# Kernel tuning notes

Measured on AMD Instinct MI355X. Metric: run time of the kernel, lower is better.

The kernel has to match this reference:

```python
import jax, jax.numpy as jnp
import numpy as np

B, N, C, H = 2, 2048, 256, 8
HD = C // H
LN_EPS = 1e-5
BN_EPS = 1e-5  # eval-mode BatchNorm with running_mean=0, running_var=1


def _ln(x, g, b):
    # LayerNorm over last dim
    m = jnp.mean(x, axis=-1, keepdims=True)
    v = jnp.mean((x - m) ** 2, axis=-1, keepdims=True)
    return (x - m) * jax.lax.rsqrt(v + LN_EPS) * g + b


def _ln_cn(x, g, b):
    # x: [B,C,N], normalize over C (torch does transpose -> LN -> transpose)
    return jnp.swapaxes(_ln(jnp.swapaxes(x, 1, 2), g, b), 1, 2)


def _cdist(a, b):
    # a: [B,N,D], b: [B,M,D] -> [B,N,M] euclidean
    d2 = (jnp.sum(a * a, -1)[:, :, None] + jnp.sum(b * b, -1)[:, None, :]
          - 2.0 * jnp.einsum('bnd,bmd->bnm', a, b))
    return jnp.sqrt(jnp.maximum(d2, 0.0))


def _conv1x1(w, x, b=None):
    # w: [O,C], x: [B,C,N]
    y = jnp.einsum('oc,bcn->bon', w, x)
    return y if b is None else y + b[None, :, None]


def setup_inputs() -> dict:
    key = jax.random.key(0)
    ks = jax.random.split(key, 32)
    s = 0.02
    inp = {
        'xyz_A': jax.random.normal(ks[0], (B, N, 3), jnp.float32),
        'featA': jax.random.normal(ks[1], (B, C, N), jnp.float32),
        'xyz_B': jax.random.normal(ks[2], (B, N, 3), jnp.float32),
        'featB': jax.random.normal(ks[3], (B, C, N), jnp.float32),
        'ln_in_g': jnp.ones((C,), jnp.float32),
        'ln_in_b': jnp.zeros((C,), jnp.float32),
        'Wq': jax.random.normal(ks[4], (C, C), jnp.float32) * s,
        'bq': jnp.zeros((C,), jnp.float32),
        'Wk': jax.random.normal(ks[5], (C, C), jnp.float32) * s,
        'bk': jnp.zeros((C,), jnp.float32),
        'Wv': jax.random.normal(ks[6], (C, C), jnp.float32) * s,
        'bv': jnp.zeros((C,), jnp.float32),
        'sb_w1': jax.random.normal(ks[7], (H // 2, 1), jnp.float32) * s,
        'sb_bn_g': jnp.ones((H // 2,), jnp.float32),
        'sb_bn_b': jnp.zeros((H // 2,), jnp.float32),
        'sb_w2': jax.random.normal(ks[8], (H, H // 2), jnp.float32) * s,
        'sb_b2': jnp.zeros((H,), jnp.float32),
        'Wqd': jax.random.normal(ks[9], (C, C), jnp.float32) * s,
        'bqd': jnp.zeros((C,), jnp.float32),
        'Wkd': jax.random.normal(ks[10], (C, C), jnp.float32) * s,
        'bkd': jnp.zeros((C,), jnp.float32),
        'ln_sim_g': jnp.ones((C,), jnp.float32),
        'ln_sim_b': jnp.zeros((C,), jnp.float32),
        'ln_dis_g': jnp.ones((C,), jnp.float32),
        'ln_dis_b': jnp.zeros((C,), jnp.float32),
        'Wf1': jax.random.normal(ks[11], (2 * C, 3 * C), jnp.float32) * s,
        'bnf_g': jnp.ones((2 * C,), jnp.float32),
        'bnf_b': jnp.zeros((2 * C,), jnp.float32),
        'Wf2': jax.random.normal(ks[12], (C, 2 * C), jnp.float32) * s,
        'bf2': jnp.zeros((C,), jnp.float32),
    }
    return inp


def reference(xyz_A, featA, xyz_B, featB, ln_in_g, ln_in_b, Wq, bq, Wk, bk, Wv, bv,
              sb_w1, sb_bn_g, sb_bn_b, sb_w2, sb_b2, Wqd, bqd, Wkd, bkd,
              ln_sim_g, ln_sim_b, ln_dis_g, ln_dis_b, Wf1, bnf_g, bnf_b, Wf2, bf2):
    featA_norm = _ln_cn(featA, ln_in_g, ln_in_b)  # [B,C,N]

    # spatial bias: cdist -> 1x1 conv2d MLP over channel dim
    dist = _cdist(xyz_A, xyz_B)  # [B,N,N]
    h = jnp.einsum('oi,binm->bonm', sb_w1, -dist[:, None])  # [B,H/2,N,N]
    h = h * (sb_bn_g / np.sqrt(1.0 + BN_EPS))[None, :, None, None] + sb_bn_b[None, :, None, None]
    h = jax.nn.relu(h)
    spatial_bias = jnp.einsum('oi,binm->bonm', sb_w2, h) + sb_b2[None, :, None, None]  # [B,H,N,N]

    # similarity path
    q = _conv1x1(Wq, featA_norm, bq).reshape(B, H, HD, N).transpose(0, 1, 3, 2)  # [B,H,N,hd]
    k = _conv1x1(Wk, featB, bk).reshape(B, H, HD, N).transpose(0, 1, 3, 2)
    sim_scores = jnp.einsum('bhnd,bhmd->bhnm', q, k) / np.sqrt(HD) + spatial_bias

    # dissimilarity path: feature-space cdist
    qd = jnp.swapaxes(_conv1x1(Wqd, featA_norm, bqd), 1, 2)  # [B,N,C]
    kd = jnp.swapaxes(_conv1x1(Wkd, featB, bkd), 1, 2)
    dissim_scores = _cdist(qd, kd)[:, None] + spatial_bias  # [B,H,N,N]

    sim_w = jax.nn.softmax(sim_scores, axis=-1)
    dis_w = jax.nn.softmax(dissim_scores, axis=-1)

    v = _conv1x1(Wv, featB, bv).reshape(B, H, HD, N).transpose(0, 1, 3, 2)  # [B,H,N,hd]
    ctx_sim = jnp.einsum('bhnm,bhmd->bhnd', sim_w, v).transpose(0, 1, 3, 2).reshape(B, C, N)
    ctx_sim = _ln_cn(ctx_sim, ln_sim_g, ln_sim_b)
    ctx_dis = jnp.einsum('bhnm,bhmd->bhnd', dis_w, v).transpose(0, 1, 3, 2).reshape(B, C, N)
    ctx_dis = _ln_cn(ctx_dis, ln_dis_g, ln_dis_b)

    fused_in = jnp.concatenate([featA_norm, ctx_sim, ctx_dis], axis=1)  # [B,3C,N]
    f = jnp.einsum('oc,bcn->bon', Wf1, fused_in)
    f = f * (bnf_g / np.sqrt(1.0 + BN_EPS))[None, :, None] + bnf_b[None, :, None]
    f = jax.nn.relu(f)
    fused = jnp.einsum('oc,bcn->bon', Wf2, f) + bf2[None, :, None]

    return fused + featA  # residual (in_channel == out_channel -> Identity)
```

## Files before the change

kernel.cpp:

```cpp
#include <hip/hip_runtime.h>
#include <math.h>

#define B_ 2
#define N_ 2048
#define C_ 256
#define H_ 8
#define HD_ 32
constexpr float LN_EPS_ = 1e-5f;
constexpr float BN_EPS_ = 1e-5f;
constexpr float LOG2E_ = 1.4426950408889634f;
constexpr float ISDL_ = 0.17677669529663687f * 1.4426950408889634f;

typedef __attribute__((ext_vector_type(8))) short bf16x8;
typedef __attribute__((ext_vector_type(4))) float f32x4;

static __device__ inline ushort f2bf(float x) {
    union { float f; uint u; } c{x};
    uint r = (c.u + 0x7FFF + ((c.u >> 16) & 1)) >> 16;
    return (ushort)r;
}
static __device__ inline float bf2f(ushort u) {
    union { uint i; float f; } c; c.i = ((uint)u) << 16; return c.f;
}
static __device__ inline float bf_lo(uint u) { return __uint_as_float(u << 16); }
static __device__ inline float bf_hi(uint u) { return __uint_as_float(u & 0xffff0000u); }
static __device__ inline float lane_bcast(float v, int srclane) {
    return __int_as_float(__builtin_amdgcn_ds_bpermute(srclane * 4, __float_as_int(v)));
}
static __device__ inline uint pack_bf2(float lo, float hi) {
    uint ul = __float_as_uint(lo) + 0x8000u;
    uint uh = __float_as_uint(hi) + 0x8000u;
    return __builtin_amdgcn_perm(uh, ul, 0x07060302u);
}

__global__ __launch_bounds__(256)
void k_wconv(const float* __restrict__ Wq, const float* __restrict__ Wqd,
             const float* __restrict__ Wk, const float* __restrict__ Wkd,
             const float* __restrict__ Wv, const float* __restrict__ Wf1,
             const float* __restrict__ Wf2, ushort* __restrict__ dst)
{
    size_t e0 = ((size_t)blockIdx.x * 256 + threadIdx.x) * 8;
    const float* src = Wq; size_t base = 0;
    if (e0 >= 65536)  { src = Wqd; base = 65536; }
    if (e0 >= 131072) { src = Wk;  base = 131072; }
    if (e0 >= 196608) { src = Wkd; base = 196608; }
    if (e0 >= 262144) { src = Wv;  base = 262144; }
    if (e0 >= 327680) { src = Wf1; base = 327680; }
    if (e0 >= 720896) { src = Wf2; base = 720896; }
    float4 a = *(const float4*)(src + (e0 - base));
    float4 b = *(const float4*)(src + (e0 - base) + 4);
    ushort o[8] = {f2bf(a.x), f2bf(a.y), f2bf(a.z), f2bf(a.w),
                   f2bf(b.x), f2bf(b.y), f2bf(b.z), f2bf(b.w)};
    *(uint4*)(dst + e0) = *(uint4*)o;
}

__global__ __launch_bounds__(512)
void k_bconcat(const float* __restrict__ bq, const float* __restrict__ bqd,
               const float* __restrict__ bk, const float* __restrict__ bkd,
               float* __restrict__ bqqd, float* __restrict__ bkkd)
{
    int t = threadIdx.x;
    bqqd[t] = (t < 256) ? bq[t] : bqd[t - 256];
    bkkd[t] = (t < 256) ? bk[t] : bkd[t - 256];
}

template<bool DO_LN>
__global__ __launch_bounds__(256)
void k_ln_transpose(const float* __restrict__ x,
                    const float* __restrict__ g,
                    const float* __restrict__ bt,
                    ushort* __restrict__ out, int ld)
{
    __shared__ float tile[C_][65];
    __shared__ float red_s[4][64];
    __shared__ float red_q[4][64];
    __shared__ float ms[64];
    __shared__ float rs[64];

    const int b  = blockIdx.x / (N_ / 64);
    const int n0 = (blockIdx.x % (N_ / 64)) * 64;
    const int tid = threadIdx.x;

    for (int i = 0; i < 64; ++i) {
        int c = i * 4 + (tid >> 6);
        int n = tid & 63;
        tile[c][n] = x[((size_t)b * C_ + c) * N_ + n0 + n];
    }
    __syncthreads();

    float gv = 0.f, bv = 0.f;
    if (DO_LN) { gv = g[tid]; bv = bt[tid]; }

    if (DO_LN) {
        const int nl = tid & 63, part = tid >> 6;
        float s = 0.f, q = 0.f;
        for (int j = 0; j < 64; ++j) {
            float v = tile[part * 64 + j][nl];
            s += v; q += v * v;
        }
        red_s[part][nl] = s; red_q[part][nl] = q;
        __syncthreads();
        if (tid < 64) {
            float ss = red_s[0][tid] + red_s[1][tid] + red_s[2][tid] + red_s[3][tid];
            float qq = red_q[0][tid] + red_q[1][tid] + red_q[2][tid] + red_q[3][tid];
            float mean = ss * (1.0f / C_);
            float var  = qq * (1.0f / C_) - mean * mean;
            ms[tid] = mean;
            rs[tid] = rsqrtf(var + LN_EPS_);
        }
        __syncthreads();
    }

    for (int i = 0; i < 64; ++i) {
        float v = tile[tid][i];
        if (DO_LN) v = (v - ms[i]) * rs[i] * gv + bv;
        out[((size_t)b * N_ + n0 + i) * ld + tid] = f2bf(v);
    }
}

template<int EPI, int OUT>
__global__ __launch_bounds__(256)
void k_gemm_bf(const ushort* __restrict__ A, int lda, size_t sAz,
               const ushort* __restrict__ Bw, int ldb, size_t sBz,
               void* __restrict__ Cout_, int ldc, size_t sCz,
               int K,
               const float* __restrict__ aux1,
               const float* __restrict__ aux2)
{
    const int z = blockIdx.z;
    A  += (size_t)z * sAz;
    Bw += (size_t)z * sBz;

    const int r0 = blockIdx.x * 64;
    const int c0 = blockIdx.y * 64;
    const int tid = threadIdx.x;
    const int w = tid >> 6, lane = tid & 63;
    const int wr = w >> 1, wc = w & 1;
    const int ql = lane & 15, g = lane >> 4;

    __shared__ ushort As[64][40];
    __shared__ ushort Bs[64][40];

    f32x4 acc[2][2] = {};
    const int srow = tid >> 2;
    const int sk   = (tid & 3) * 8;

    for (int k0 = 0; k0 < K; k0 += 32) {
        bf16x8 av = *(const bf16x8*)&A[(size_t)(r0 + srow) * lda + k0 + sk];
        bf16x8 bv = *(const bf16x8*)&Bw[(size_t)(c0 + srow) * ldb + k0 + sk];
        __syncthreads();
        *(bf16x8*)&As[srow][sk] = av;
        *(bf16x8*)&Bs[srow][sk] = bv;
        __syncthreads();
        bf16x8 af[2], bf[2];
        #pragma unroll
        for (int i = 0; i < 2; ++i) {
            af[i] = *(const bf16x8*)&As[wr * 32 + i * 16 + ql][8 * g];
            bf[i] = *(const bf16x8*)&Bs[wc * 32 + i * 16 + ql][8 * g];
        }
        #pragma unroll
        for (int mi = 0; mi < 2; ++mi)
            #pragma unroll
            for (int ni = 0; ni < 2; ++ni)
                acc[mi][ni] = __builtin_amdgcn_mfma_f32_16x16x32_bf16(af[mi], bf[ni], acc[mi][ni], 0, 0, 0);
    }

    const float inv_bn = rsqrtf(1.0f + BN_EPS_);
    float*  Cf = (float*)Cout_  + (size_t)z * sCz;
    ushort* Cb = (ushort*)Cout_ + (size_t)z * sCz;
    #pragma unroll
    for (int mi = 0; mi < 2; ++mi) {
        #pragma unroll
        for (int ni = 0; ni < 2; ++ni) {
            #pragma unroll
            for (int r = 0; r < 4; ++r) {
                int row = r0 + wr * 32 + mi * 16 + 4 * g + r;
                int col = c0 + wc * 32 + ni * 16 + ql;
                float v = acc[mi][ni][r];
                if (EPI == 0) {
                    v += aux1[col];
                } else if (EPI == 1) {
                    float qnv = aux1[(size_t)z * N_ + row];
                    float knv = aux2[(size_t)z * N_ + col];
                    v = sqrtf(fmaxf(qnv + knv - 2.0f * v, 0.f)) * LOG2E_;
                } else if (EPI == 2) {
                    v = fmaxf(v * (aux1[col] * inv_bn) + aux2[col], 0.f);
                } else if (EPI == 3) {
                    v += aux1[row];
                }
                if (OUT == 0) Cf[(size_t)row * ldc + col] = v;
                else          Cb[(size_t)row * ldc + col] = f2bf(v);
            }
        }
    }
}

__global__ __launch_bounds__(256)
void k_rownorm(const ushort* __restrict__ x, int ld, float* __restrict__ outn)
{
    const int r = blockIdx.x * 4 + (threadIdx.x >> 6);
    const int lane = threadIdx.x & 63;
    uint2 pv = *(const uint2*)&x[(size_t)r * ld + lane * 4];
    float v0 = bf2f((ushort)(pv.x & 0xffff)), v1 = bf2f((ushort)(pv.x >> 16));
    float v2 = bf2f((ushort)(pv.y & 0xffff)), v3 = bf2f((ushort)(pv.y >> 16));
    float s = v0 * v0 + v1 * v1 + v2 * v2 + v3 * v3;
    #pragma unroll
    for (int off = 32; off; off >>= 1) s += __shfl_xor(s, off);
    if (lane == 0) outn[r] = s;
}

#define QLD_ 512
__global__ __launch_bounds__(512, 4)
void k_attn7(const ushort* __restrict__ q_bf,
             const ushort* __restrict__ k_bf,
             const ushort* __restrict__ v_c,
             const float* __restrict__ xyzA,
             const float* __restrict__ xyzB,
             const ushort* __restrict__ cdb,
             const float* __restrict__ sb_w1, const float* __restrict__ sb_bn_g,
             const float* __restrict__ sb_bn_b, const float* __restrict__ sb_w2,
             const float* __restrict__ sb_b2,
             ushort* __restrict__ pc,
             float* __restrict__ pml)
{
    __shared__ ushort biasL[2][4][16][72];
    __shared__ ushort cdsL[2][16][72];
    __shared__ ushort ps[8][16][72];
    __shared__ float  w2Ls[4][4];
    __shared__ float  b2Ls[4];

    const int n0 = blockIdx.x * 16;
    const int b  = blockIdx.y;
    const int hg   = blockIdx.z & 1;
    const int half = blockIdx.z >> 1;
    const size_t bN = (size_t)b * N_;
    const int tid = threadIdx.x;
    const int w = tid >> 6, lane = tid & 63;
    const int path = w >> 2, hl = w & 3;
    const int h = hg * 4 + hl;
    const int ql = lane & 15, g = lane >> 4;

    if (tid < 4) {
        b2Ls[tid] = sb_b2[hg * 4 + tid] * LOG2E_;
        #pragma unroll
        for (int i = 0; i < 4; ++i) w2Ls[tid][i] = sb_w2[(hg * 4 + tid) * 4 + i] * LOG2E_;
    }

    const float inv_bn = rsqrtf(1.0f + BN_EPS_);
    float w1s_[4], bnb_[4];
    #pragma unroll
    for (int i = 0; i < 4; ++i) {
        w1s_[i] = sb_w1[i] * sb_bn_g[i] * inv_bn;
        bnb_[i] = sb_bn_b[i];
    }

    const int cq = tid >> 5, cm2 = tid & 31;
    const float ax = xyzA[(bN + n0 + cq) * 3 + 0];
    const float ay = xyzA[(bN + n0 + cq) * 3 + 1];
    const float az = xyzA[(bN + n0 + cq) * 3 + 2];

    bf16x8 qfrag = {};
    if (path == 0)
        qfrag = *(const bf16x8*)&q_bf[(bN + n0 + ql) * QLD_ + h * 32 + 8 * g];

    float m_i = -INFINITY, l_i = 0.f;
    f32x4 ctx0 = {0.f, 0.f, 0.f, 0.f};
    f32x4 ctx1 = {0.f, 0.f, 0.f, 0.f};
    const f32x4 zf = {0.f, 0.f, 0.f, 0.f};

    const int tBeg = half * (N_ / 128);
    const int tEnd = tBeg + (N_ / 128);

    float xb[6]; uint cdv;
    auto coop_load = [&](int t) {
        const int mA = t * 64 + 2 * cm2;
        const float* pb = xyzB + (bN + mA) * 3;
        #pragma unroll
        for (int i = 0; i < 6; ++i) xb[i] = pb[i];
        cdv = *(const uint*)&cdb[(bN + n0 + cq) * (size_t)N_ + mA];
    };
    auto coop_write = [&](int buf) {
        float dx0 = ax - xb[0], dy0 = ay - xb[1], dz0 = az - xb[2];
        float dx1 = ax - xb[3], dy1 = ay - xb[4], dz1 = az - xb[5];
        float d0 = sqrtf(dx0 * dx0 + dy0 * dy0 + dz0 * dz0);
        float d1 = sqrtf(dx1 * dx1 + dy1 * dy1 + dz1 * dz1);
        float f0[4], f1[4];
        #pragma unroll
        for (int i = 0; i < 4; ++i) {
            f0[i] = fmaxf(fmaf(-w1s_[i], d0, bnb_[i]), 0.f);
            f1[i] = fmaxf(fmaf(-w1s_[i], d1, bnb_[i]), 0.f);
        }
        #pragma unroll
        for (int hh = 0; hh < 4; ++hh) {
            const f32x4 w2v = *(const f32x4*)w2Ls[hh];
            float b0 = b2Ls[hh], b1 = b2Ls[hh];
            #pragma unroll
            for (int i = 0; i < 4; ++i) {
                b0 = fmaf(w2v[i], f0[i], b0);
                b1 = fmaf(w2v[i], f1[i], b1);
            }
            *(uint*)&biasL[buf][hh][cq][2 * cm2] = pack_bf2(b0, b1);
        }
        *(uint*)&cdsL[buf][cq][2 * cm2] = cdv;
    };

    __syncthreads();
    coop_load(tBeg);
    coop_write(0);
    if (tBeg + 1 < tEnd) coop_load(tBeg + 1);
    __syncthreads();

    for (int t = tBeg; t < tEnd; ++t) {
        const int cur = (t - tBeg) & 1;

        if (t + 1 < tEnd) {
            coop_write(cur ^ 1);
            if (t + 2 < tEnd) coop_load(t + 2);
        }

        const int m0 = t * 64;
        bf16x8 af[4];
        if (path == 0) {
            #pragma unroll
            for (int mt = 0; mt < 4; ++mt)
                af[mt] = *(const bf16x8*)&k_bf[(bN + m0 + mt * 16 + ql) * QLD_ + h * 32 + 8 * g];
        }
        bf16x8 vb[2][2];
        #pragma unroll
        for (int kb = 0; kb < 2; ++kb)
            #pragma unroll
            for (int dt = 0; dt < 2; ++dt)
                vb[kb][dt] = *(const bf16x8*)&v_c[((size_t)b * C_ + h * 32 + dt * 16 + ql) * N_ + m0 + kb * 32 + 8 * g];

        float s[16];
        #pragma unroll
        for (int mt = 0; mt < 4; ++mt) {
            uint2 bw = *(const uint2*)&biasL[cur][hl][ql][16 * mt + 4 * g];
            s[4 * mt + 0] = bf_lo(bw.x);
            s[4 * mt + 1] = bf_hi(bw.x);
            s[4 * mt + 2] = bf_lo(bw.y);
            s[4 * mt + 3] = bf_hi(bw.y);
        }

        if (path == 0) {
            __builtin_amdgcn_s_setprio(1);
            #pragma unroll
            for (int mt = 0; mt < 4; ++mt) {
                f32x4 sf = __builtin_amdgcn_mfma_f32_16x16x32_bf16(af[mt], qfrag, zf, 0, 0, 0);
                #pragma unroll
                for (int r = 0; r < 4; ++r)
                    s[4 * mt + r] = fmaf(sf[r], ISDL_, s[4 * mt + r]);
            }
            __builtin_amdgcn_s_setprio(0);
        } else {
            #pragma unroll
            for (int mt = 0; mt < 4; ++mt) {
                uint2 cw = *(const uint2*)&cdsL[cur][ql][16 * mt + 4 * g];
                s[4 * mt + 0] += bf_lo(cw.x);
                s[4 * mt + 1] += bf_hi(cw.x);
                s[4 * mt + 2] += bf_lo(cw.y);
                s[4 * mt + 3] += bf_hi(cw.y);
            }
        }

        float t0 = fmaxf(s[0], s[1]),   t1 = fmaxf(s[2], s[3]);
        float t2 = fmaxf(s[4], s[5]),   t3 = fmaxf(s[6], s[7]);
        float t4 = fmaxf(s[8], s[9]),   t5 = fmaxf(s[10], s[11]);
        float t6 = fmaxf(s[12], s[13]), t7 = fmaxf(s[14], s[15]);
        t0 = fmaxf(t0, t1); t2 = fmaxf(t2, t3);
        t4 = fmaxf(t4, t5); t6 = fmaxf(t6, t7);
        float tmax = fmaxf(fmaxf(t0, t2), fmaxf(t4, t6));
        tmax = fmaxf(tmax, __shfl_xor(tmax, 16));
        tmax = fmaxf(tmax, __shfl_xor(tmax, 32));
        if (!__all(tmax <= m_i + 8.0f)) {
            float mnew = fmaxf(m_i, tmax);
            float scl = exp2f(m_i - mnew);
            l_i *= scl;
            #pragma unroll
            for (int r = 0; r < 4; ++r) {
                float sr = lane_bcast(scl, 4 * g + r);
                ctx0[r] *= sr; ctx1[r] *= sr;
            }
            m_i = mnew;
        }
        float lsum = 0.f;
        #pragma unroll
        for (int j = 0; j < 16; ++j) {
            float pj = exp2f(s[j] - m_i);
            s[j] = pj;
            lsum += pj;
        }
        lsum += __shfl_xor(lsum, 16);
        lsum += __shfl_xor(lsum, 32);
        l_i += lsum;

        #pragma unroll
        for (int mt = 0; mt < 4; ++mt) {
            uint2 pk;
            pk.x = pack_bf2(s[4 * mt + 0], s[4 * mt + 1]);
            pk.y = pack_bf2(s[4 * mt + 2], s[4 * mt + 3]);
            *(uint2*)&ps[w][ql][16 * mt + 4 * g] = pk;
        }

        __builtin_amdgcn_s_setprio(1);
        #pragma unroll
        for (int kb = 0; kb < 2; ++kb) {
            bf16x8 pa = *(const bf16x8*)&ps[w][ql][kb * 32 + 8 * g];
            ctx0 = __builtin_amdgcn_mfma_f32_16x16x32_bf16(pa, vb[kb][0], ctx0, 0, 0, 0);
            ctx1 = __builtin_amdgcn_mfma_f32_16x16x32_bf16(pa, vb[kb][1], ctx1, 0, 0, 0);
        }
        __builtin_amdgcn_s_setprio(0);

        __syncthreads();
    }

    const size_t sl = (size_t)(half * 2 + path) * (B_ * N_);
    #pragma unroll
    for (int r = 0; r < 4; ++r) {
        size_t base = (sl + bN + n0 + 4 * g + r) * C_ + h * 32;
        pc[base + ql]      = f2bf(ctx0[r]);
        pc[base + 16 + ql] = f2bf(ctx1[r]);
    }
    if (g == 0) {
        size_t mlb = ((sl + bN + n0 + ql) * H_ + h) * 2;
        pml[mlb]     = m_i;
        pml[mlb + 1] = l_i;
    }
}

__global__ __launch_bounds__(256)
void k_merge_ln(const ushort* __restrict__ pc, const float* __restrict__ pml,
                const float* __restrict__ g_sim, const float* __restrict__ b_sim,
                const float* __restrict__ g_dis, const float* __restrict__ b_dis,
                ushort* __restrict__ fused_bf)
{
    __shared__ float rs_[4], rq_[4];
    const int row = blockIdx.x;
    const int path = blockIdx.y;
    const int c = threadIdx.x;
    const int h = c >> 5;
    const size_t i0 = (size_t)(0 * 2 + path) * (B_ * N_) + row;
    const size_t i1 = (size_t)(1 * 2 + path) * (B_ * N_) + row;
    const float m0 = pml[(i0 * H_ + h) * 2], l0 = pml[(i0 * H_ + h) * 2 + 1];
    const float m1 = pml[(i1 * H_ + h) * 2], l1 = pml[(i1 * H_ + h) * 2 + 1];
    const float M = fmaxf(m0, m1);
    const float w0 = exp2f(m0 - M), w1 = exp2f(m1 - M);
    const float il = 1.0f / fmaf(l0, w0, l1 * w1);
    const float v = fmaf(bf2f(pc[i0 * C_ + c]), w0, bf2f(pc[i1 * C_ + c]) * w1) * il;

    float s = v, q = v * v;
    #pragma unroll
    for (int off = 32; off; off >>= 1) { s += __shfl_xor(s, off); q += __shfl_xor(q, off); }
    const int wv = c >> 6, lane = c & 63;
    if (lane == 0) { rs_[wv] = s; rq_[wv] = q; }
    __syncthreads();
    float ss = rs_[0] + rs_[1] + rs_[2] + rs_[3];
    float qq = rq_[0] + rq_[1] + rq_[2] + rq_[3];
    float mean = ss * (1.0f / C_);
    float var  = qq * (1.0f / C_) - mean * mean;
    float rstd = rsqrtf(var + LN_EPS_);
    const float* gp = path ? g_dis : g_sim;
    const float* bp = path ? b_dis : b_sim;
    fused_bf[(size_t)row * (3 * C_) + C_ + path * C_ + c] =
        f2bf((v - mean) * rstd * gp[c] + bp[c]);
}

__global__ __launch_bounds__(256)
void k_transpose_add(const float* __restrict__ fused_t,
                     const float* __restrict__ featA,
                     float* __restrict__ out)
{
    __shared__ float t[64][65];
    const int n0 = blockIdx.x * 64, c0 = blockIdx.y * 64, b = blockIdx.z;
    const int tid = threadIdx.x;
    #pragma unroll
    for (int i = 0; i < 16; ++i) {
        int e = i * 256 + tid;
        int nn = e >> 6, cc = e & 63;
        t[nn][cc] = fused_t[((size_t)b * N_ + n0 + nn) * C_ + c0 + cc];
    }
    __syncthreads();
    #pragma unroll
    for (int i = 0; i < 16; ++i) {
        int e = i * 256 + tid;
        int cc = e >> 6, nn = e & 63;
        size_t idx = ((size_t)b * C_ + c0 + cc) * N_ + n0 + nn;
        out[idx] = t[nn][cc] + featA[idx];
    }
}

extern "C" void kernel_launch(void* const* d_in, const int* in_sizes, int n_in,
                              void* d_out, int out_size, void* d_ws, size_t ws_size,
                              hipStream_t stream)
{
    const float* xyz_A   = (const float*)d_in[0];
    const float* featA   = (const float*)d_in[1];
    const float* xyz_B   = (const float*)d_in[2];
    const float* featB   = (const float*)d_in[3];
    const float* ln_in_g = (const float*)d_in[4];
    const float* ln_in_b = (const float*)d_in[5];
    const float* Wq  = (const float*)d_in[6];
    const float* bq  = (const float*)d_in[7];
    const float* Wk  = (const float*)d_in[8];
    const float* bk  = (const float*)d_in[9];
    const float* Wv  = (const float*)d_in[10];
    const float* bv  = (const float*)d_in[11];
    const float* sb_w1   = (const float*)d_in[12];
    const float* sb_bn_g = (const float*)d_in[13];
    const float* sb_bn_b = (const float*)d_in[14];
    const float* sb_w2   = (const float*)d_in[15];
    const float* sb_b2   = (const float*)d_in[16];
    const float* Wqd = (const float*)d_in[17];
    const float* bqd = (const float*)d_in[18];
    const float* Wkd = (const float*)d_in[19];
    const float* bkd = (const float*)d_in[20];
    const float* ln_sim_g = (const float*)d_in[21];
    const float* ln_sim_b = (const float*)d_in[22];
    const float* ln_dis_g = (const float*)d_in[23];
    const float* ln_dis_b = (const float*)d_in[24];
    const float* Wf1   = (const float*)d_in[25];
    const float* bnf_g = (const float*)d_in[26];
    const float* bnf_b = (const float*)d_in[27];
    const float* Wf2   = (const float*)d_in[28];
    const float* bf2   = (const float*)d_in[29];
    float* out = (float*)d_out;

    float* ws = (float*)d_ws;
    size_t off = 0;
    auto alloc = [&](size_t n) { float* p = ws + off; off += n; return p; };
    const size_t RN = (size_t)B_ * N_;

    ushort* fused_bf = (ushort*)alloc(RN * 384);
    ushort* featB_bf = (ushort*)alloc(RN * 128);
    ushort* qqd_bf   = (ushort*)alloc(RN * 256);
    ushort* kkd_bf   = (ushort*)alloc(RN * 256);
    ushort* v_bf     = (ushort*)alloc(RN * 128);
    ushort* wbf      = (ushort*)alloc(425984);
    float*  bqqd     = alloc(512);
    float*  bkkd     = alloc(512);
    float*  qn       = alloc(RN);
    float*  kn       = alloc(RN);
    ushort* cd_bf    = (ushort*)alloc((size_t)B_ * N_ * N_ / 2);
    ushort* pc       = (ushort*)alloc(4 * RN * C_ / 2);
    float*  pml      = alloc(4 * RN * H_ * 2);

    ushort* q_bf  = qqd_bf;
    ushort* qd_bf = qqd_bf + 256;
    ushort* k_bf  = kkd_bf;
    ushort* kd_bf = kkd_bf + 256;
    ushort* fh      = cd_bf;
    float*  fused_t = (float*)(cd_bf + (size_t)RN * 512);

    ushort* wqqd_bf = wbf;
    ushort* wkkd_bf = wbf + 131072;
    ushort* wv_bf   = wbf + 262144;
    ushort* wf1_bf  = wbf + 327680;
    ushort* wf2_bf  = wbf + 720896;
    (void)ws_size; (void)in_sizes; (void)n_in; (void)out_size;

    dim3 blk(256);

    k_wconv<<<dim3(416), blk, 0, stream>>>(Wq, Wqd, Wk, Wkd, Wv, Wf1, Wf2, wbf);
    k_bconcat<<<dim3(1), dim3(512), 0, stream>>>(bq, bqd, bk, bkd, bqqd, bkkd);
    k_ln_transpose<true ><<<dim3(B_ * (N_ / 64)), blk, 0, stream>>>(featA, ln_in_g, ln_in_b, fused_bf, 3 * C_);
    k_ln_transpose<false><<<dim3(B_ * (N_ / 64)), blk, 0, stream>>>(featB, nullptr, nullptr, featB_bf, C_);

    k_gemm_bf<0,1><<<dim3(RN / 64, 8, 1), blk, 0, stream>>>(fused_bf, 3 * C_, 0, wqqd_bf, C_, 0, qqd_bf, 512, 0, C_, bqqd, nullptr);
    k_gemm_bf<0,1><<<dim3(RN / 64, 8, 1), blk, 0, stream>>>(featB_bf, C_,     0, wkkd_bf, C_, 0, kkd_bf, 512, 0, C_, bkkd, nullptr);
    k_gemm_bf<3,1><<<dim3(C_ / 64, N_ / 64, B_), blk, 0, stream>>>(wv_bf, C_, 0, featB_bf, C_, (size_t)N_ * C_, v_bf, N_, (size_t)C_ * N_, C_, bv, nullptr);

    k_rownorm<<<dim3(RN / 4), blk, 0, stream>>>(qd_bf, 512, qn);
    k_rownorm<<<dim3(RN / 4), blk, 0, stream>>>(kd_bf, 512, kn);
    k_gemm_bf<1,1><<<dim3(N_ / 64, N_ / 64, B_), blk, 0, stream>>>(qd_bf, 512, (size_t)N_ * 512,
                                                                   kd_bf, 512, (size_t)N_ * 512,
                                                                   cd_bf, N_, (size_t)N_ * N_, C_, qn, kn);

    k_attn7<<<dim3(N_ / 16, B_, 4), dim3(512), 0, stream>>>(q_bf, k_bf, v_bf, xyz_A, xyz_B, cd_bf,
                                                            sb_w1, sb_bn_g, sb_bn_b, sb_w2, sb_b2,
                                                            pc, pml);
    k_merge_ln<<<dim3(RN, 2), blk, 0, stream>>>(pc, pml, ln_sim_g, ln_sim_b, ln_dis_g, ln_dis_b, fused_bf);

    k_gemm_bf<2,1><<<dim3(RN / 64, 8, 1), blk, 0, stream>>>(fused_bf, 3 * C_, 0, wf1_bf, 3 * C_, 0, fh, 2 * C_, 0, 3 * C_, bnf_g, bnf_b);
    k_gemm_bf<0,0><<<dim3(RN / 64, 4, 1), blk, 0, stream>>>(fh, 2 * C_, 0, wf2_bf, 2 * C_, 0, fused_t, C_, 0, 2 * C_, bf2, nullptr);

    k_transpose_add<<<dim3(N_ / 64, C_ / 64, B_), blk, 0, stream>>>(fused_t, featA, out);
}
```

Baseline: 204.8 us.

## Process 32 query rows per attention block to reuse K/V fragments

The attention kernel now covers 32 query rows per block instead of 16. Each wave keeps two query fragments and two sets of online-softmax state, so every K and V fragment loaded from global memory feeds twice as many MFMAs. Shared-memory tiles double in row count, and the coop loader now computes four spatial-bias entries per thread. The grid is halved, and register and LDS pressure rise, which may lower occupancy and block-level parallelism.

```diff
diff --git a/kernel.cpp b/kernel.cpp
--- a/kernel.cpp
+++ b/kernel.cpp
@@ -211,7 +211,7 @@
 
 #define QLD_ 512
 __global__ __launch_bounds__(512, 4)
-void k_attn7(const ushort* __restrict__ q_bf,
+void k_attn8(const ushort* __restrict__ q_bf,
              const ushort* __restrict__ k_bf,
              const ushort* __restrict__ v_c,
              const float* __restrict__ xyzA,
@@ -223,13 +223,13 @@
              ushort* __restrict__ pc,
              float* __restrict__ pml)
 {
-    __shared__ ushort biasL[2][4][16][72];
-    __shared__ ushort cdsL[2][16][72];
-    __shared__ ushort ps[8][16][72];
+    __shared__ ushort biasL[2][4][32][68];
+    __shared__ ushort cdsL[2][32][68];
+    __shared__ ushort ps[8][32][68];
     __shared__ float  w2Ls[4][4];
     __shared__ float  b2Ls[4];
 
-    const int n0 = blockIdx.x * 16;
+    const int n0 = blockIdx.x * 32;
     const int b  = blockIdx.y;
     const int hg   = blockIdx.z & 1;
     const int half = blockIdx.z >> 1;
@@ -254,59 +254,72 @@
         bnb_[i] = sb_bn_b[i];
     }
 
-    const int cq = tid >> 5, cm2 = tid & 31;
+    const int cq = tid >> 4, mp = tid & 15;
     const float ax = xyzA[(bN + n0 + cq) * 3 + 0];
     const float ay = xyzA[(bN + n0 + cq) * 3 + 1];
     const float az = xyzA[(bN + n0 + cq) * 3 + 2];
 
-    bf16x8 qfrag = {};
-    if (path == 0)
-        qfrag = *(const bf16x8*)&q_bf[(bN + n0 + ql) * QLD_ + h * 32 + 8 * g];
-
-    float m_i = -INFINITY, l_i = 0.f;
-    f32x4 ctx0 = {0.f, 0.f, 0.f, 0.f};
-    f32x4 ctx1 = {0.f, 0.f, 0.f, 0.f};
+    bf16x8 qf0 = {}, qf1 = {};
+    if (path == 0) {
+        qf0 = *(const bf16x8*)&q_bf[(bN + n0 + ql) * QLD_ + h * 32 + 8 * g];
+        qf1 = *(const bf16x8*)&q_bf[(bN + n0 + 16 + ql) * QLD_ + h * 32 + 8 * g];
+    }
+
+    float m0_ = -INFINITY, l0_ = 0.f, m1_ = -INFINITY, l1_ = 0.f;
+    f32x4 c00 = {0,0,0,0}, c01 = {0,0,0,0};
+    f32x4 c10 = {0,0,0,0}, c11 = {0,0,0,0};
     const f32x4 zf = {0.f, 0.f, 0.f, 0.f};
 
     const int tBeg = half * (N_ / 128);
     const int tEnd = tBeg + (N_ / 128);
 
-    float xb[6]; uint cdv;
+    uint cdv0, cdv1;
     auto coop_load = [&](int t) {
-        const int mA = t * 64 + 2 * cm2;
-        const float* pb = xyzB + (bN + mA) * 3;
-        #pragma unroll
-        for (int i = 0; i < 6; ++i) xb[i] = pb[i];
-        cdv = *(const uint*)&cdb[(bN + n0 + cq) * (size_t)N_ + mA];
+        const size_t rb = (bN + n0 + cq) * (size_t)N_ + t * 64;
+        cdv0 = *(const uint*)&cdb[rb + 2 * mp];
+        cdv1 = *(const uint*)&cdb[rb + 2 * mp + 32];
     };
-    auto coop_write = [&](int buf) {
-        float dx0 = ax - xb[0], dy0 = ay - xb[1], dz0 = az - xb[2];
-        float dx1 = ax - xb[3], dy1 = ay - xb[4], dz1 = az - xb[5];
-        float d0 = sqrtf(dx0 * dx0 + dy0 * dy0 + dz0 * dz0);
-        float d1 = sqrtf(dx1 * dx1 + dy1 * dy1 + dz1 * dz1);
-        float f0[4], f1[4];
-        #pragma unroll
-        for (int i = 0; i < 4; ++i) {
-            f0[i] = fmaxf(fmaf(-w1s_[i], d0, bnb_[i]), 0.f);
-            f1[i] = fmaxf(fmaf(-w1s_[i], d1, bnb_[i]), 0.f);
-        }
+    auto coop_write = [&](int buf, int t) {
+        const size_t mBase = bN + t * 64;
+        const float* p0 = xyzB + (mBase + 2 * mp) * 3;
+        const float* p1 = xyzB + (mBase + 2 * mp + 32) * 3;
+        float d[4];
+        {
+            float dx = ax - p0[0], dy = ay - p0[1], dz = az - p0[2];
+            d[0] = sqrtf(dx * dx + dy * dy + dz * dz);
+            dx = ax - p0[3]; dy = ay - p0[4]; dz = az - p0[5];
+            d[1] = sqrtf(dx * dx + dy * dy + dz * dz);
+            dx = ax - p1[0]; dy = ay - p1[1]; dz = az - p1[2];
+            d[2] = sqrtf(dx * dx + dy * dy + dz * dz);
+            dx = ax - p1[3]; dy = ay - p1[4]; dz = az - p1[5];
+            d[3] = sqrtf(dx * dx + dy * dy + dz * dz);
+        }
+        float f[4][4];
+        #pragma unroll
+        for (int e = 0; e < 4; ++e)
+            #pragma unroll
+            for (int i = 0; i < 4; ++i)
+                f[e][i] = fmaxf(fmaf(-w1s_[i], d[e], bnb_[i]), 0.f);
         #pragma unroll
         for (int hh = 0; hh < 4; ++hh) {
             const f32x4 w2v = *(const f32x4*)w2Ls[hh];
-            float b0 = b2Ls[hh], b1 = b2Ls[hh];
-            #pragma unroll
-            for (int i = 0; i < 4; ++i) {
-                b0 = fmaf(w2v[i], f0[i], b0);
-                b1 = fmaf(w2v[i], f1[i], b1);
+            float bb[4];
+            #pragma unroll
+            for (int e = 0; e < 4; ++e) {
+                bb[e] = b2Ls[hh];
+                #pragma unroll
+                for (int i = 0; i < 4; ++i) bb[e] = fmaf(w2v[i], f[e][i], bb[e]);
             }
-            *(uint*)&biasL[buf][hh][cq][2 * cm2] = pack_bf2(b0, b1);
-        }
-        *(uint*)&cdsL[buf][cq][2 * cm2] = cdv;
+            *(uint*)&biasL[buf][hh][cq][2 * mp]      = pack_bf2(bb[0], bb[1]);
+            *(uint*)&biasL[buf][hh][cq][2 * mp + 32] = pack_bf2(bb[2], bb[3]);
+        }
+        *(uint*)&cdsL[buf][cq][2 * mp]      = cdv0;
+        *(uint*)&cdsL[buf][cq][2 * mp + 32] = cdv1;
     };
 
     __syncthreads();
     coop_load(tBeg);
-    coop_write(0);
+    coop_write(0, tBeg);
     if (tBeg + 1 < tEnd) coop_load(tBeg + 1);
     __syncthreads();
 
@@ -314,7 +327,7 @@
         const int cur = (t - tBeg) & 1;
 
         if (t + 1 < tEnd) {
-            coop_write(cur ^ 1);
+            coop_write(cur ^ 1, t + 1);
             if (t + 2 < tEnd) coop_load(t + 2);
         }
 
@@ -332,82 +345,106 @@
             for (int dt = 0; dt < 2; ++dt)
                 vb[kb][dt] = *(const bf16x8*)&v_c[((size_t)b * C_ + h * 32 + dt * 16 + ql) * N_ + m0 + kb * 32 + 8 * g];
 
-        float s[16];
+        float s0[16], s1[16];
         #pragma unroll
         for (int mt = 0; mt < 4; ++mt) {
-            uint2 bw = *(const uint2*)&biasL[cur][hl][ql][16 * mt + 4 * g];
-            s[4 * mt + 0] = bf_lo(bw.x);
-            s[4 * mt + 1] = bf_hi(bw.x);
-            s[4 * mt + 2] = bf_lo(bw.y);
-            s[4 * mt + 3] = bf_hi(bw.y);
+            uint2 bw0 = *(const uint2*)&biasL[cur][hl][ql][16 * mt + 4 * g];
+            uint2 bw1 = *(const uint2*)&biasL[cur][hl][16 + ql][16 * mt + 4 * g];
+            s0[4 * mt + 0] = bf_lo(bw0.x); s0[4 * mt + 1] = bf_hi(bw0.x);
+            s0[4 * mt + 2] = bf_lo(bw0.y); s0[4 * mt + 3] = bf_hi(bw0.y);
+            s1[4 * mt + 0] = bf_lo(bw1.x); s1[4 * mt + 1] = bf_hi(bw1.x);
+            s1[4 * mt + 2] = bf_lo(bw1.y); s1[4 * mt + 3] = bf_hi(bw1.y);
         }
 
         if (path == 0) {
             __builtin_amdgcn_s_setprio(1);
             #pragma unroll
             for (int mt = 0; mt < 4; ++mt) {
-                f32x4 sf = __builtin_amdgcn_mfma_f32_16x16x32_bf16(af[mt], qfrag, zf, 0, 0, 0);
+                f32x4 sf0 = __builtin_amdgcn_mfma_f32_16x16x32_bf16(af[mt], qf0, zf, 0, 0, 0);
+                f32x4 sf1 = __builtin_amdgcn_mfma_f32_16x16x32_bf16(af[mt], qf1, zf, 0, 0, 0);
                 #pragma unroll
-                for (int r = 0; r < 4; ++r)
-                    s[4 * mt + r] = fmaf(sf[r], ISDL_, s[4 * mt + r]);
+                for (int r = 0; r < 4; ++r) {
+                    s0[4 * mt + r] = fmaf(sf0[r], ISDL_, s0[4 * mt + r]);
+                    s1[4 * mt + r] = fmaf(sf1[r], ISDL_, s1[4 * mt + r]);
+                }
             }
             __builtin_amdgcn_s_setprio(0);
         } else {
             #pragma unroll
             for (int mt = 0; mt < 4; ++mt) {
-                uint2 cw = *(const uint2*)&cdsL[cur][ql][16 * mt + 4 * g];
-                s[4 * mt + 0] += bf_lo(cw.x);
-                s[4 * mt + 1] += bf_hi(cw.x);
-                s[4 * mt + 2] += bf_lo(cw.y);
-                s[4 * mt + 3] += bf_hi(cw.y);
+                uint2 c0w = *(const uint2*)&cdsL[cur][ql][16 * mt + 4 * g];
+                uint2 c1w = *(const uint2*)&cdsL[cur][16 + ql][16 * mt + 4 * g];
+                s0[4 * mt + 0] += bf_lo(c0w.x); s0[4 * mt + 1] += bf_hi(c0w.x);
+                s0[4 * mt + 2] += bf_lo(c0w.y); s0[4 * mt + 3] += bf_hi(c0w.y);
+                s1[4 * mt + 0] += bf_lo(c1w.x); s1[4 * mt + 1] += bf_hi(c1w.x);
+                s1[4 * mt + 2] += bf_lo(c1w.y); s1[4 * mt + 3] += bf_hi(c1w.y);
             }
         }
 
-        float t0 = fmaxf(s[0], s[1]),   t1 = fmaxf(s[2], s[3]);
-        float t2 = fmaxf(s[4], s[5]),   t3 = fmaxf(s[6], s[7]);
-        float t4 = fmaxf(s[8], s[9]),   t5 = fmaxf(s[10], s[11]);
-        float t6 = fmaxf(s[12], s[13]), t7 = fmaxf(s[14], s[15]);
-        t0 = fmaxf(t0, t1); t2 = fmaxf(t2, t3);
-        t4 = fmaxf(t4, t5); t6 = fmaxf(t6, t7);
-        float tmax = fmaxf(fmaxf(t0, t2), fmaxf(t4, t6));
-        tmax = fmaxf(tmax, __shfl_xor(tmax, 16));
-        tmax = fmaxf(tmax, __shfl_xor(tmax, 32));
-        if (!__all(tmax <= m_i + 8.0f)) {
-            float mnew = fmaxf(m_i, tmax);
-            float scl = exp2f(m_i - mnew);
-            l_i *= scl;
+        float tmax0, tmax1;
+        {
+            float a0 = fmaxf(fmaxf(s0[0], s0[1]), fmaxf(s0[2], s0[3]));
+            float a1 = fmaxf(fmaxf(s0[4], s0[5]), fmaxf(s0[6], s0[7]));
+            float a2 = fmaxf(fmaxf(s0[8], s0[9]), fmaxf(s0[10], s0[11]));
+            float a3 = fmaxf(fmaxf(s0[12], s0[13]), fmaxf(s0[14], s0[15]));
+            tmax0 = fmaxf(fmaxf(a0, a1), fmaxf(a2, a3));
+            float b0v = fmaxf(fmaxf(s1[0], s1[1]), fmaxf(s1[2], s1[3]));
+            float b1v = fmaxf(fmaxf(s1[4], s1[5]), fmaxf(s1[6], s1[7]));
+            float b2v = fmaxf(fmaxf(s1[8], s1[9]), fmaxf(s1[10], s1[11]));
+            float b3v = fmaxf(fmaxf(s1[12], s1[13]), fmaxf(s1[14], s1[15]));
+            tmax1 = fmaxf(fmaxf(b0v, b1v), fmaxf(b2v, b3v));
+        }
+        tmax0 = fmaxf(tmax0, __shfl_xor(tmax0, 16));
+        tmax0 = fmaxf(tmax0, __shfl_xor(tmax0, 32));
+        tmax1 = fmaxf(tmax1, __shfl_xor(tmax1, 16));
+        tmax1 = fmaxf(tmax1, __shfl_xor(tmax1, 32));
+        if (!__all((tmax0 <= m0_ + 8.0f) && (tmax1 <= m1_ + 8.0f))) {
+            float mn0 = fmaxf(m0_, tmax0);
+            float mn1 = fmaxf(m1_, tmax1);
+            float sc0 = exp2f(m0_ - mn0);
+            float sc1 = exp2f(m1_ - mn1);
+            l0_ *= sc0; l1_ *= sc1;
             #pragma unroll
             for (int r = 0; r < 4; ++r) {
-                float sr = lane_bcast(scl, 4 * g + r);
-                ctx0[r] *= sr; ctx1[r] *= sr;
+                float sr0 = lane_bcast(sc0, 4 * g + r);
+                float sr1 = lane_bcast(sc1, 4 * g + r);
+                c00[r] *= sr0; c01[r] *= sr0;
+                c10[r] *= sr1; c11[r] *= sr1;
             }
-            m_i = mnew;
-        }
-        float lsum = 0.f;
+            m0_ = mn0; m1_ = mn1;
+        }
+        float ls0 = 0.f, ls1 = 0.f;
         #pragma unroll
         for (int j = 0; j < 16; ++j) {
-            float pj = exp2f(s[j] - m_i);
-            s[j] = pj;
-            lsum += pj;
-        }
-        lsum += __shfl_xor(lsum, 16);
-        lsum += __shfl_xor(lsum, 32);
-        l_i += lsum;
+            float p0 = exp2f(s0[j] - m0_);
+            float p1 = exp2f(s1[j] - m1_);
+            s0[j] = p0; s1[j] = p1;
+            ls0 += p0; ls1 += p1;
+        }
+        ls0 += __shfl_xor(ls0, 16); ls0 += __shfl_xor(ls0, 32);
+        ls1 += __shfl_xor(ls1, 16); ls1 += __shfl_xor(ls1, 32);
+        l0_ += ls0; l1_ += ls1;
 
         #pragma unroll
         for (int mt = 0; mt < 4; ++mt) {
-            uint2 pk;
-            pk.x = pack_bf2(s[4 * mt + 0], s[4 * mt + 1]);
-            pk.y = pack_bf2(s[4 * mt + 2], s[4 * mt + 3]);
-            *(uint2*)&ps[w][ql][16 * mt + 4 * g] = pk;
+            uint2 pk0, pk1;
+            pk0.x = pack_bf2(s0[4 * mt + 0], s0[4 * mt + 1]);
+            pk0.y = pack_bf2(s0[4 * mt + 2], s0[4 * mt + 3]);
+            pk1.x = pack_bf2(s1[4 * mt + 0], s1[4 * mt + 1]);
+            pk1.y = pack_bf2(s1[4 * mt + 2], s1[4 * mt + 3]);
+            *(uint2*)&ps[w][ql][16 * mt + 4 * g]      = pk0;
+            *(uint2*)&ps[w][16 + ql][16 * mt + 4 * g] = pk1;
         }
 
         __builtin_amdgcn_s_setprio(1);
         #pragma unroll
         for (int kb = 0; kb < 2; ++kb) {
-            bf16x8 pa = *(const bf16x8*)&ps[w][ql][kb * 32 + 8 * g];
-            ctx0 = __builtin_amdgcn_mfma_f32_16x16x32_bf16(pa, vb[kb][0], ctx0, 0, 0, 0);
-            ctx1 = __builtin_amdgcn_mfma_f32_16x16x32_bf16(pa, vb[kb][1], ctx1, 0, 0, 0);
+            bf16x8 pa0 = *(const bf16x8*)&ps[w][ql][kb * 32 + 8 * g];
+            bf16x8 pa1 = *(const bf16x8*)&ps[w][16 + ql][kb * 32 + 8 * g];
+            c00 = __builtin_amdgcn_mfma_f32_16x16x32_bf16(pa0, vb[kb][0], c00, 0, 0, 0);
+            c01 = __builtin_amdgcn_mfma_f32_16x16x32_bf16(pa0, vb[kb][1], c01, 0, 0, 0);
+            c10 = __builtin_amdgcn_mfma_f32_16x16x32_bf16(pa1, vb[kb][0], c10, 0, 0, 0);
+            c11 = __builtin_amdgcn_mfma_f32_16x16x32_bf16(pa1, vb[kb][1], c11, 0, 0, 0);
         }
         __builtin_amdgcn_s_setprio(0);
 
@@ -417,14 +454,20 @@
     const size_t sl = (size_t)(half * 2 + path) * (B_ * N_);
     #pragma unroll
     for (int r = 0; r < 4; ++r) {
-        size_t base = (sl + bN + n0 + 4 * g + r) * C_ + h * 32;
-        pc[base + ql]      = f2bf(ctx0[r]);
-        pc[base + 16 + ql] = f2bf(ctx1[r]);
+        size_t b0 = (sl + bN + n0 + 4 * g + r) * C_ + h * 32;
+        pc[b0 + ql]      = f2bf(c00[r]);
+        pc[b0 + 16 + ql] = f2bf(c01[r]);
+        size_t b1 = (sl + bN + n0 + 16 + 4 * g + r) * C_ + h * 32;
+        pc[b1 + ql]      = f2bf(c10[r]);
+        pc[b1 + 16 + ql] = f2bf(c11[r]);
     }
     if (g == 0) {
-        size_t mlb = ((sl + bN + n0 + ql) * H_ + h) * 2;
-        pml[mlb]     = m_i;
-        pml[mlb + 1] = l_i;
+        size_t mlb0 = ((sl + bN + n0 + ql) * H_ + h) * 2;
+        pml[mlb0]     = m0_;
+        pml[mlb0 + 1] = l0_;
+        size_t mlb1 = ((sl + bN + n0 + 16 + ql) * H_ + h) * 2;
+        pml[mlb1]     = m1_;
+        pml[mlb1 + 1] = l1_;
     }
 }
 
@@ -575,7 +618,7 @@
                                                                    kd_bf, 512, (size_t)N_ * 512,
                                                                    cd_bf, N_, (size_t)N_ * N_, C_, qn, kn);
 
-    k_attn7<<<dim3(N_ / 16, B_, 4), dim3(512), 0, stream>>>(q_bf, k_bf, v_bf, xyz_A, xyz_B, cd_bf,
+    k_attn8<<<dim3(N_ / 32, B_, 4), dim3(512), 0, stream>>>(q_bf, k_bf, v_bf, xyz_A, xyz_B, cd_bf,
                                                             sb_w1, sb_bn_g, sb_bn_b, sb_w2, sb_b2,
                                                             pc, pml);
     k_merge_ln<<<dim3(RN, 2), blk, 0, stream>>>(pc, pml, ln_sim_g, ln_sim_b, ln_dis_g, ln_dis_b, fused_bf);
```

Result: slower. 225.7 us (+10.2%).
